# Optimization experiments

Measured on AMD Instinct MI355X. Metric: run time of the kernel, lower is better.

The kernel has to match this reference:

```python
import jax, jax.numpy as jnp
import numpy as np

Q_LO, Q_HI = 0.15, 0.85   # quantiles from __init__ q=(0.15, 0.85)
Z_INDEX = 0.0             # Z_index=0 -> mask = outside [q_lo, q_hi]
Z_SIMPLE = 1.0            # Z_index_simple fallback


def _nn_diff(S1, S2):
    # For each point in S1, signed per-coordinate residual to its nearest
    # neighbor in S2 (brute-force cdist + argmin + gather). S1:[N,3] S2:[M,3]
    d2 = (jnp.sum(S1 * S1, -1)[:, None] + jnp.sum(S2 * S2, -1)[None, :]
          - 2.0 * (S1 @ S2.T))              # [N, M] squared distances
    idx = jnp.argmin(d2, axis=1)            # nearest index in S2, [N]
    return S1 - S2[idx]                     # [N, 3]


def _robust_masked_std(x):
    # torch: quantile-based outlier mask (no_grad), then unbiased std of
    # the masked elements. Implemented with mask weights so shapes are static.
    xf = x.reshape(-1)
    xs = jax.lax.stop_gradient(xf)
    qs = jnp.quantile(xs, jnp.array([Q_LO, Q_HI], dtype=xs.dtype))
    iqr = qs[1] - qs[0]
    mask = (xs < qs[0] - Z_INDEX * iqr) | (xs > qs[1] + Z_INDEX * iqr)
    # fallback chain matching torch edge cases: simple |x-mean|>Z*std, then all
    mu, sd = xs.mean(), xs.std(ddof=1)
    simple = jnp.abs(xs - mu) > Z_SIMPLE * sd
    simple = jnp.where(simple.sum() > 0, simple, jnp.ones_like(simple))
    w = jnp.where(mask.sum() > 0, mask, simple).astype(xf.dtype)
    cnt = w.sum()
    mean_w = jnp.sum(w * xf) / cnt
    var = jnp.sum(w * (xf - mean_w) ** 2) / (cnt - 1.0)  # unbiased (torch.std)
    return jnp.sqrt(var)


def _sigma_max(S1, S2):
    s1 = _robust_masked_std(_nn_diff(S1, S2))  # std of S1->S2 residuals
    s2 = _robust_masked_std(_nn_diff(S2, S1))  # std of S2->S1 residuals
    return jnp.maximum(s1, s2)                 # max(self.sigma_distance(...))


def setup_inputs() -> dict:
    key = jax.random.key(0)
    k1, k2 = jax.random.split(key)
    B, N, M, D = 16, 4096, 4096, 3
    x = jax.random.uniform(k1, (B, N, D), dtype=jnp.float32)
    y = jax.random.uniform(k2, (B, M, D), dtype=jnp.float32)
    return {"x": x, "y": y}


def reference(x, y):
    per_batch = jax.vmap(_sigma_max)(x, y)  # [B]
    return per_batch.mean()
```

## Files before the change

kernel.cpp:

```cpp
#include <hip/hip_runtime.h>
#include <stdint.h>
#include <math.h>

typedef unsigned short u16;
typedef unsigned long long ull;

#define NPTS  4096
#define NB    16
#define NRES  12288
#define NPAIR 32
#define G     16
#define NCELL 4096
#define HCEL  0.0625f
#define SSTR  4160
#define MARGIN 1e-5f
#define RANK_LO 1843u
#define RANK_HI 10443u

__device__ __forceinline__ uint32_t f2key(float f) {
    uint32_t u = __float_as_uint(f);
    return (u & 0x80000000u) ? ~u : (u | 0x80000000u);
}
__device__ __forceinline__ float key2f(uint32_t k) {
    uint32_t u = (k & 0x80000000u) ? (k ^ 0x80000000u) : ~k;
    return __uint_as_float(u);
}

__global__ __launch_bounds__(1024) void build_kernel(const float* __restrict__ x,
                                                     const float* __restrict__ y,
                                                     float4* __restrict__ arrA,
                                                     u16* __restrict__ starts,
                                                     unsigned int* __restrict__ counters) {
    __shared__ uint32_t hist[NCELL];
    __shared__ uint32_t wpart[16];
    const int pd = blockIdx.x, b = pd >> 1, dir = pd & 1;
    const float* t = (dir == 0 ? y : x) + (size_t)b * NPTS * 3;
    const int tid = threadIdx.x, lane = tid & 63, wv = tid >> 6;

    #pragma unroll
    for (int j = 0; j < 4; ++j) hist[tid * 4 + j] = 0u;
    if (pd == 0 && tid == 0) counters[0] = 0u;
    __syncthreads();

    float f[12];
    int ci[4];
    {
        const float4* tp = reinterpret_cast<const float4*>(t + (size_t)tid * 12);
        #pragma unroll
        for (int j = 0; j < 3; ++j) {
            const float4 v = tp[j];
            f[j * 4 + 0] = v.x; f[j * 4 + 1] = v.y; f[j * 4 + 2] = v.z; f[j * 4 + 3] = v.w;
        }
        #pragma unroll
        for (int k = 0; k < 4; ++k) {
            const int cx = (int)(f[k * 3 + 0] * 16.f);
            const int cy = (int)(f[k * 3 + 1] * 16.f);
            const int cz = (int)(f[k * 3 + 2] * 16.f);
            ci[k] = (cx * G + cy) * G + cz;
            atomicAdd(&hist[ci[k]], 1u);
        }
    }
    __syncthreads();

    {
        uint32_t loc[4], sum = 0;
        const int base = tid * 4;
        #pragma unroll
        for (int j = 0; j < 4; ++j) { loc[j] = hist[base + j]; sum += loc[j]; }
        uint32_t sc = sum;
        #pragma unroll
        for (int off = 1; off < 64; off <<= 1) {
            const uint32_t u = __shfl_up(sc, off);
            if (lane >= off) sc += u;
        }
        if (lane == 63) wpart[wv] = sc;
        __syncthreads();
        uint32_t wbase = 0;
        #pragma unroll
        for (int k = 0; k < 16; ++k) wbase += (k < wv) ? wpart[k] : 0u;
        uint32_t ex = wbase + sc - sum;
        #pragma unroll
        for (int j = 0; j < 4; ++j) { hist[base + j] = ex; ex += loc[j]; }
    }
    __syncthreads();

    for (int i = tid; i <= NCELL; i += 1024)
        starts[(size_t)pd * SSTR + i] = (u16)((i == NCELL) ? NPTS : hist[i]);
    __syncthreads();

    #pragma unroll
    for (int k = 0; k < 4; ++k) {
        const float px = f[k * 3 + 0], py = f[k * 3 + 1], pz = f[k * 3 + 2];
        const uint32_t pos = atomicAdd(&hist[ci[k]], 1u);
        const float w = fmaf(pz, pz, fmaf(py, py, px * px));
        arrA[(size_t)pd * NPTS + pos] = make_float4(-2.f * px, -2.f * py, -2.f * pz, w);
    }
}

__global__ __launch_bounds__(256, 8) void query_kernel(const float4* __restrict__ arrA,
                                                       const u16* __restrict__ starts,
                                                       uint32_t* __restrict__ keys,
                                                       double* __restrict__ partials) {
    __shared__ double wred[8];
    const int pd = blockIdx.y;
    const int tid = threadIdx.x, lane = tid & 63, wv = tid >> 6;
    const int l4 = tid & 3;
    const int p = blockIdx.x * 64 + (tid >> 2);

    const float4* __restrict__ tp = arrA + (size_t)pd * NPTS;
    const u16* __restrict__ st = starts + (size_t)pd * SSTR;

    const float4 Q = arrA[(size_t)(pd ^ 1) * NPTS + p];
    const float qx = -0.5f * Q.x, qy = -0.5f * Q.y, qz = -0.5f * Q.z;
    const float qq = Q.w;
    const int cx = (int)(qx * 16.f), cy = (int)(qy * 16.f), cz = (int)(qz * 16.f);

    ull pk = ~0ull;

    {
        const int zlo = max(cz - 1, 0), zhi = min(cz + 1, G - 1);
        #define RUNB(RR, AV, NV)                                                  \
            int AV, NV;                                                           \
            { const int ix = min(max(cx + (RR) / 3 - 1, 0), G - 1);               \
              const int iy = min(max(cy + (RR) % 3 - 1, 0), G - 1);               \
              const int cc = (ix * G + iy) * G;                                   \
              AV = st[cc + zlo];                                                  \
              NV = st[cc + zhi + 1] - AV; }
        RUNB(0, a0, n0) RUNB(1, a1, n1) RUNB(2, a2, n2)
        RUNB(3, a3, n3) RUNB(4, a4, n4) RUNB(5, a5, n5)
        RUNB(6, a6, n6) RUNB(7, a7, n7) RUNB(8, a8, n8)
        #undef RUNB
        const int nc = n0 + n1 + n2 + n3 + n4 + n5 + n6 + n7 + n8;

        for (int li = l4; li < nc; li += 4) {
            int pos;
            {
                int rem = li; pos = a0 + rem;
                rem -= n0; pos = (rem >= 0) ? a1 + rem : pos;
                rem -= n1; pos = (rem >= 0) ? a2 + rem : pos;
                rem -= n2; pos = (rem >= 0) ? a3 + rem : pos;
                rem -= n3; pos = (rem >= 0) ? a4 + rem : pos;
                rem -= n4; pos = (rem >= 0) ? a5 + rem : pos;
                rem -= n5; pos = (rem >= 0) ? a6 + rem : pos;
                rem -= n6; pos = (rem >= 0) ? a7 + rem : pos;
                rem -= n7; pos = (rem >= 0) ? a8 + rem : pos;
                pos = min(pos, NPTS - 1);
            }
            const float4 T = tp[pos];
            const float d = fmaf(qx, T.x, fmaf(qy, T.y, fmaf(qz, T.z, T.w)));
            const ull cand = ((ull)f2key(d) << 32) | (uint32_t)pos;
            pk = (cand < pk) ? cand : pk;
        }
    }

    {
        ull o = __shfl_xor(pk, 1); pk = (o < pk) ? o : pk;
        o = __shfl_xor(pk, 2);     pk = (o < pk) ? o : pk;
    }

    for (int s = 2; s <= G - 1; ++s) {
        const float bd = key2f((uint32_t)(pk >> 32));
        const float dmin = (float)(s - 1) * HCEL;
        if (fmaf(dmin, dmin, -(bd + qq)) > MARGIN) break;
        for (int dx = -s; dx <= s; ++dx) {
            const int ix = cx + dx;
            if (ix < 0 || ix > G - 1) continue;
            const int adx = dx < 0 ? -dx : dx;
            for (int dy = -s; dy <= s; ++dy) {
                const int iy = cy + dy;
                if (iy < 0 || iy > G - 1) continue;
                const int ady = dy < 0 ? -dy : dy;
                const int c0 = (ix * G + iy) * G;
                #define SCANS(A_, E_)                                                 \
                    for (int p2 = (A_) + l4; p2 < (E_); p2 += 4) {                    \
                        const float4 T = tp[p2];                                      \
                        const float d = fmaf(qx, T.x, fmaf(qy, T.y,                   \
                                             fmaf(qz, T.z, T.w)));                    \
                        const ull cand = ((ull)f2key(d) << 32) | (uint32_t)p2;        \
                        pk = (cand < pk) ? cand : pk;                                 \
                    }
                if (max(adx, ady) == s) {
                    const int zl = max(cz - s, 0), zh = min(cz + s, G - 1);
                    const int a = st[c0 + zl], e = st[c0 + zh + 1];
                    SCANS(a, e)
                } else {
                    const int z1 = cz - s;
                    if (z1 >= 0) { const int a = st[c0 + z1], e = st[c0 + z1 + 1]; SCANS(a, e) }
                    const int z2 = cz + s;
                    if (z2 <= G - 1) { const int a = st[c0 + z2], e = st[c0 + z2 + 1]; SCANS(a, e) }
                }
                #undef SCANS
            }
        }
        ull o = __shfl_xor(pk, 1); pk = (o < pk) ? o : pk;
        o = __shfl_xor(pk, 2);     pk = (o < pk) ? o : pk;
    }

    const int pos = (int)(uint32_t)pk;
    const float4 T = tp[pos];
    const float rx = qx - (-0.5f * T.x);
    const float ry = qy - (-0.5f * T.y);
    const float rz = qz - (-0.5f * T.z);

    if (l4 < 3) {
        const uint32_t kk = (l4 == 0) ? f2key(rx) : ((l4 == 1) ? f2key(ry) : f2key(rz));
        keys[(size_t)pd * NRES + (size_t)p * 3 + l4] = kk;
    }

    double s1 = 0.0, s2 = 0.0;
    if (l4 == 0) {
        s1 = (double)rx + (double)ry + (double)rz;
        s2 = (double)rx * rx + (double)ry * ry + (double)rz * rz;
    }
    #pragma unroll
    for (int off = 32; off; off >>= 1) { s1 += __shfl_down(s1, off); s2 += __shfl_down(s2, off); }
    if (lane == 0) { wred[wv] = s1; wred[4 + wv] = s2; }
    __syncthreads();
    if (tid == 0) {
        double a = 0.0, c = 0.0;
        for (int k = 0; k < 4; ++k) { a += wred[k]; c += wred[4 + k]; }
        partials[(size_t)pd * 128 + blockIdx.x + 0]  = a;
        partials[(size_t)pd * 128 + 64 + blockIdx.x] = c;
    }
}

template <int BPT>
__device__ __forceinline__ void scanB(uint32_t* h, uint32_t* wtmp) {
    const int tid = threadIdx.x, lane = tid & 63, wv = tid >> 6;
    const int base = tid * BPT;
    uint32_t loc[BPT], sum = 0;
    #pragma unroll
    for (int j = 0; j < BPT; ++j) { loc[j] = h[base + j]; sum += loc[j]; }
    uint32_t sc = sum;
    #pragma unroll
    for (int off = 1; off < 64; off <<= 1) {
        const uint32_t u = __shfl_up(sc, off);
        if (lane >= off) sc += u;
    }
    if (lane == 63) wtmp[wv] = sc;
    __syncthreads();
    uint32_t wb = 0;
    #pragma unroll
    for (int k = 0; k < 16; ++k) wb += (k < wv) ? wtmp[k] : 0u;
    uint32_t ex = wb + sc - sum;
    #pragma unroll
    for (int j = 0; j < BPT; ++j) { h[base + j] = ex; ex += loc[j]; }
    __syncthreads();
}

template <int BPT>
__device__ __forceinline__ void psearchB(const uint32_t* h, int n, uint32_t r,
                                         uint32_t total, uint32_t* out3) {
    const int base = threadIdx.x * BPT;
    #pragma unroll
    for (int j = 0; j < BPT; ++j) {
        const int i = base + j;
        if (i < n) {
            const uint32_t lo = h[i];
            const uint32_t hi = (i + 1 < n) ? h[i + 1] : total;
            if (lo <= r && r < hi) { out3[0] = (uint32_t)i; out3[1] = lo; out3[2] = hi; }
        }
    }
}

__global__ __launch_bounds__(1024) void sigma_kernel(const uint32_t* __restrict__ keysg,
                                                     const double* __restrict__ partials,
                                                     float* __restrict__ sig,
                                                     unsigned int* __restrict__ counters,
                                                     float* __restrict__ out) {
    __shared__ uint32_t hist[4096];
    __shared__ uint32_t wtmp[16];
    __shared__ uint32_t bc[12];
    __shared__ double dr[64];
    __shared__ int io[32];
    __shared__ uint32_t um[32];

    const int pair = blockIdx.x;
    const int tid = threadIdx.x, lane = tid & 63, wv = tid >> 6;

    uint32_t key[12];
    const uint32_t* kp = keysg + (size_t)pair * NRES;
    #pragma unroll
    for (int e = 0; e < 12; ++e) key[e] = kp[e * 1024 + tid];

    {
        double a = (tid < 128) ? partials[(size_t)pair * 128 + tid] : 0.0;
        #pragma unroll
        for (int off = 32; off; off >>= 1) a += __shfl_down(a, off);
        if (lane == 0 && wv < 2) dr[wv] = a;
    }
    __syncthreads();
    const double S = dr[0], S2 = dr[1];
    const double mu = S / NRES;
    const double var_all = (S2 - S * mu) / (NRES - 1);
    const double sd = sqrt(var_all > 0.0 ? var_all : 0.0);
    __syncthreads();

    hist[tid * 2] = 0u; hist[tid * 2 + 1] = 0u;
    __syncthreads();
    #pragma unroll
    for (int e = 0; e < 12; ++e) atomicAdd(&hist[key[e] >> 21], 1u);
    __syncthreads();
    scanB<2>(hist, wtmp);
    psearchB<2>(hist, 2048, RANK_LO, NRES, bc + 0);
    psearchB<2>(hist, 2048, RANK_HI, NRES, bc + 3);
    __syncthreads();
    const uint32_t pA1 = bc[0], rA1 = RANK_LO - bc[1], totA1 = bc[2] - bc[1];
    const uint32_t pB1 = bc[3], rB1 = RANK_HI - bc[4], totB1 = bc[5] - bc[4];
    __syncthreads();

    #pragma unroll
    for (int j = 0; j < 4; ++j) hist[tid * 4 + j] = 0u;
    __syncthreads();
    #pragma unroll
    for (int e = 0; e < 12; ++e) {
        const uint32_t k = key[e];
        const uint32_t pfx = k >> 21, bin = (k >> 10) & 2047u;
        if (pfx == pA1) atomicAdd(&hist[bin], 1u);
        if (pfx == pB1) atomicAdd(&hist[2048 + bin], 1u);
    }
    __syncthreads();
    scanB<2>(hist, wtmp);
    scanB<2>(hist + 2048, wtmp);
    psearchB<2>(hist, 2048, rA1, totA1, bc + 0);
    psearchB<2>(hist + 2048, 2048, rB1, totB1, bc + 3);
    __syncthreads();
    const uint32_t pA2 = (pA1 << 11) | bc[0], rA2 = rA1 - bc[1], totA2 = bc[2] - bc[1];
    const uint32_t pB2 = (pB1 << 11) | bc[3], rB2 = rB1 - bc[4], totB2 = bc[5] - bc[4];
    __syncthreads();

    hist[tid * 2] = 0u; hist[tid * 2 + 1] = 0u;
    __syncthreads();
    #pragma unroll
    for (int e = 0; e < 12; ++e) {
        const uint32_t k = key[e];
        if ((k >> 10) == pA2) atomicAdd(&hist[k & 1023u], 1u);
        if ((k >> 10) == pB2) atomicAdd(&hist[1024 + (k & 1023u)], 1u);
    }
    __syncthreads();
    scanB<1>(hist, wtmp);
    scanB<1>(hist + 1024, wtmp);
    psearchB<1>(hist, 1024, rA2, totA2, bc + 0);
    psearchB<1>(hist + 1024, 1024, rB2, totB2, bc + 3);
    __syncthreads();
    const uint32_t k0 = (pA2 << 10) | bc[0];
    const uint32_t k2 = (pB2 << 10) | bc[3];
    const bool dup1 = (bc[2] >= rA2 + 2u);
    const bool dup3 = (bc[5] >= rB2 + 2u);

    uint32_t m1 = 0xFFFFFFFFu, m3 = 0xFFFFFFFFu;
    #pragma unroll
    for (int e = 0; e < 12; ++e) {
        const uint32_t k = key[e];
        if (k > k0 && k < m1) m1 = k;
        if (k > k2 && k < m3) m3 = k;
    }
    {
        uint32_t a = m1, c = m3;
        #pragma unroll
        for (int off = 32; off; off >>= 1) {
            const uint32_t ua = __shfl_down(a, off), uc = __shfl_down(c, off);
            a = (ua < a) ? ua : a; c = (uc < c) ? uc : c;
        }
        if (lane == 0) { um[wv] = a; um[16 + wv] = c; }
    }
    __syncthreads();
    uint32_t m1r = 0xFFFFFFFFu, m3r = 0xFFFFFFFFu;
    for (int k = 0; k < 16; ++k) {
        m1r = (um[k] < m1r) ? um[k] : m1r;
        m3r = (um[16 + k] < m3r) ? um[16 + k] : m3r;
    }
    const uint32_t k1 = dup1 ? k0 : m1r;
    const uint32_t k3 = dup3 ? k2 : m3r;

    const double vl0 = (double)key2f(k0), vl1 = (double)key2f(k1);
    const double vh0 = (double)key2f(k2), vh1 = (double)key2f(k3);
    const double fr_lo = 0.15 * (NRES - 1) - (double)RANK_LO;
    const double fr_hi = 0.85 * (NRES - 1) - (double)RANK_HI;
    const float q_lo = (float)(vl0 + fr_lo * (vl1 - vl0));
    const float q_hi = (float)(vh0 + fr_hi * (vh1 - vh0));

    int cq = 0, cs = 0;
    double sq = 0.0, ss = 0.0, sqq = 0.0, ssq = 0.0;
    #pragma unroll
    for (int e = 0; e < 12; ++e) {
        const float f = key2f(key[e]);
        const double fd = (double)f;
        if ((f < q_lo) || (f > q_hi)) { cq++; sq += fd; sqq += fd * fd; }
        if (fabs(fd - mu) > sd)       { cs++; ss += fd; ssq += fd * fd; }
    }
    {
        double a0 = sq, a1 = ss, a2 = sqq, a3 = ssq;
        int b0 = cq, b1 = cs;
        #pragma unroll
        for (int off = 32; off; off >>= 1) {
            a0 += __shfl_down(a0, off); a1 += __shfl_down(a1, off);
            a2 += __shfl_down(a2, off); a3 += __shfl_down(a3, off);
            b0 += __shfl_down(b0, off); b1 += __shfl_down(b1, off);
        }
        if (lane == 0) {
            dr[wv] = a0; dr[16 + wv] = a1; dr[32 + wv] = a2; dr[48 + wv] = a3;
            io[wv] = b0; io[16 + wv] = b1;
        }
    }
    __syncthreads();
    if (tid == 0) {
        double sq_t = 0, ss_t = 0, sqq_t = 0, ssq_t = 0;
        int cq_t = 0, cs_t = 0;
        for (int k = 0; k < 16; ++k) {
            sq_t += dr[k]; ss_t += dr[16 + k]; sqq_t += dr[32 + k]; ssq_t += dr[48 + k];
            cq_t += io[k]; cs_t += io[16 + k];
        }
        double cnt, sum, sumsq;
        if (cq_t > 0)      { cnt = cq_t;  sum = sq_t; sumsq = sqq_t; }
        else if (cs_t > 0) { cnt = cs_t;  sum = ss_t; sumsq = ssq_t; }
        else               { cnt = NRES;  sum = S;    sumsq = S2; }
        const double mean_w = sum / cnt;
        const double var = (sumsq - cnt * mean_w * mean_w) / (cnt - 1.0);
        const float sv = (float)sqrt(var > 0.0 ? var : 0.0);

        __hip_atomic_store(&sig[pair], sv, __ATOMIC_RELEASE, __HIP_MEMORY_SCOPE_AGENT);
        const unsigned prev = __hip_atomic_fetch_add(&counters[0], 1u,
                                                     __ATOMIC_ACQ_REL,
                                                     __HIP_MEMORY_SCOPE_AGENT);
        if (prev == NPAIR - 1) {
            float m = 0.f;
            for (int i = 0; i < NB; ++i) {
                const float s0 = __hip_atomic_load(&sig[2 * i], __ATOMIC_ACQUIRE,
                                                   __HIP_MEMORY_SCOPE_AGENT);
                const float s1v = __hip_atomic_load(&sig[2 * i + 1], __ATOMIC_ACQUIRE,
                                                    __HIP_MEMORY_SCOPE_AGENT);
                m += fmaxf(s0, s1v);
            }
            out[0] = m / (float)NB;
        }
    }
}

extern "C" void kernel_launch(void* const* d_in, const int* in_sizes, int n_in,
                              void* d_out, int out_size, void* d_ws, size_t ws_size,
                              hipStream_t stream) {
    const float* x = (const float*)d_in[0];
    const float* y = (const float*)d_in[1];
    char* w = (char*)d_ws;
    float4*       arrA     = (float4*)(w);
    uint32_t*     keys     = (uint32_t*)(w + 2097152);
    double*       partials = (double*)(w + 3670016);
    float*        sig      = (float*)(w + 3702784);
    unsigned int* counters = (unsigned int*)(w + 3702912);
    u16*          starts   = (u16*)(w + 3703040);

    build_kernel<<<NPAIR, 1024, 0, stream>>>(x, y, arrA, starts, counters);
    query_kernel<<<dim3(64, NPAIR), 256, 0, stream>>>(arrA, starts, keys, partials);
    sigma_kernel<<<NPAIR, 1024, 0, stream>>>(keys, partials, sig, counters,
                                             (float*)d_out);
}
```

Baseline: 109.0 us.

## Fuse grid build, NN query and sigma selection into one LDS-resident kernel

```diff
diff --git a/kernel.cpp b/kernel.cpp
--- a/kernel.cpp
+++ b/kernel.cpp
@@ -12,11 +12,18 @@
 #define G     16
 #define NCELL 4096
 #define HCEL  0.0625f
-#define SSTR  4160
 #define MARGIN 1e-5f
 #define RANK_LO 1843u
 #define RANK_HI 10443u
 
+#define OFF_TGT   0
+#define OFF_CST   65536
+#define OFF_KBUF  73856
+#define OFF_DM    123008
+#define OFF_UM    123776
+#define OFF_IM    124032
+#define SMEM_SZ   124160
+
 __device__ __forceinline__ uint32_t f2key(float f) {
     uint32_t u = __float_as_uint(f);
     return (u & 0x80000000u) ? ~u : (u | 0x80000000u);
@@ -26,29 +33,75 @@
     return __uint_as_float(u);
 }
 
-__global__ __launch_bounds__(1024) void build_kernel(const float* __restrict__ x,
+template <int BPT>
+__device__ __forceinline__ void scanB(uint32_t* h, uint32_t* wtmp) {
+    const int tid = threadIdx.x, lane = tid & 63, wv = tid >> 6;
+    const int base = tid * BPT;
+    uint32_t loc[BPT], sum = 0;
+    #pragma unroll
+    for (int j = 0; j < BPT; ++j) { loc[j] = h[base + j]; sum += loc[j]; }
+    uint32_t sc = sum;
+    #pragma unroll
+    for (int off = 1; off < 64; off <<= 1) {
+        const uint32_t u = __shfl_up(sc, off);
+        if (lane >= off) sc += u;
+    }
+    if (lane == 63) wtmp[wv] = sc;
+    __syncthreads();
+    uint32_t wb = 0;
+    #pragma unroll
+    for (int k = 0; k < 16; ++k) wb += (k < wv) ? wtmp[k] : 0u;
+    uint32_t ex = wb + sc - sum;
+    #pragma unroll
+    for (int j = 0; j < BPT; ++j) { h[base + j] = ex; ex += loc[j]; }
+    __syncthreads();
+}
+
+template <int BPT>
+__device__ __forceinline__ void psearchB(const uint32_t* h, int n, uint32_t r,
+                                         uint32_t total, uint32_t* out3) {
+    const int base = threadIdx.x * BPT;
+    #pragma unroll
+    for (int j = 0; j < BPT; ++j) {
+        const int i = base + j;
+        if (i < n) {
+            const uint32_t lo = h[i];
+            const uint32_t hi = (i + 1 < n) ? h[i + 1] : total;
+            if (lo <= r && r < hi) { out3[0] = (uint32_t)i; out3[1] = lo; out3[2] = hi; }
+        }
+    }
+}
+
+__global__ __launch_bounds__(1024) void fused_kernel(const float* __restrict__ x,
                                                      const float* __restrict__ y,
-                                                     float4* __restrict__ arrA,
-                                                     u16* __restrict__ starts,
-                                                     unsigned int* __restrict__ counters) {
-    __shared__ uint32_t hist[NCELL];
-    __shared__ uint32_t wpart[16];
+                                                     float* __restrict__ sig,
+                                                     unsigned int* __restrict__ counter,
+                                                     float* __restrict__ out) {
+    __shared__ __align__(16) char smem[SMEM_SZ];
+    float4*   tgt  = (float4*)(smem + OFF_TGT);
+    u16*      cst  = (u16*)(smem + OFF_CST);
+    uint32_t* kbuf = (uint32_t*)(smem + OFF_KBUF);
+    double*   dm   = (double*)(smem + OFF_DM);
+    uint32_t* um   = (uint32_t*)(smem + OFF_UM);
+    int*      im   = (int*)(smem + OFF_IM);
+
     const int pd = blockIdx.x, b = pd >> 1, dir = pd & 1;
-    const float* t = (dir == 0 ? y : x) + (size_t)b * NPTS * 3;
+    const float* tg = (dir == 0 ? y : x) + (size_t)b * NPTS * 3;
+    const float* qg = (dir == 0 ? x : y) + (size_t)b * NPTS * 3;
     const int tid = threadIdx.x, lane = tid & 63, wv = tid >> 6;
 
+    uint32_t* hist = kbuf;
     #pragma unroll
     for (int j = 0; j < 4; ++j) hist[tid * 4 + j] = 0u;
-    if (pd == 0 && tid == 0) counters[0] = 0u;
     __syncthreads();
 
     float f[12];
     int ci[4];
     {
-        const float4* tp = reinterpret_cast<const float4*>(t + (size_t)tid * 12);
+        const float4* tp4 = reinterpret_cast<const float4*>(tg + (size_t)tid * 12);
         #pragma unroll
         for (int j = 0; j < 3; ++j) {
-            const float4 v = tp[j];
+            const float4 v = tp4[j];
             f[j * 4 + 0] = v.x; f[j * 4 + 1] = v.y; f[j * 4 + 2] = v.z; f[j * 4 + 3] = v.w;
         }
         #pragma unroll
@@ -61,287 +114,188 @@
         }
     }
     __syncthreads();
-
-    {
-        uint32_t loc[4], sum = 0;
-        const int base = tid * 4;
-        #pragma unroll
-        for (int j = 0; j < 4; ++j) { loc[j] = hist[base + j]; sum += loc[j]; }
-        uint32_t sc = sum;
-        #pragma unroll
-        for (int off = 1; off < 64; off <<= 1) {
-            const uint32_t u = __shfl_up(sc, off);
-            if (lane >= off) sc += u;
-        }
-        if (lane == 63) wpart[wv] = sc;
-        __syncthreads();
-        uint32_t wbase = 0;
-        #pragma unroll
-        for (int k = 0; k < 16; ++k) wbase += (k < wv) ? wpart[k] : 0u;
-        uint32_t ex = wbase + sc - sum;
-        #pragma unroll
-        for (int j = 0; j < 4; ++j) { hist[base + j] = ex; ex += loc[j]; }
-    }
-    __syncthreads();
-
+    scanB<4>(hist, um);
     for (int i = tid; i <= NCELL; i += 1024)
-        starts[(size_t)pd * SSTR + i] = (u16)((i == NCELL) ? NPTS : hist[i]);
-    __syncthreads();
-
+        cst[i] = (u16)((i == NCELL) ? NPTS : hist[i]);
+    __syncthreads();
     #pragma unroll
     for (int k = 0; k < 4; ++k) {
         const float px = f[k * 3 + 0], py = f[k * 3 + 1], pz = f[k * 3 + 2];
         const uint32_t pos = atomicAdd(&hist[ci[k]], 1u);
         const float w = fmaf(pz, pz, fmaf(py, py, px * px));
-        arrA[(size_t)pd * NPTS + pos] = make_float4(-2.f * px, -2.f * py, -2.f * pz, w);
-    }
-}
-
-__global__ __launch_bounds__(256, 8) void query_kernel(const float4* __restrict__ arrA,
-                                                       const u16* __restrict__ starts,
-                                                       uint32_t* __restrict__ keys,
-                                                       double* __restrict__ partials) {
-    __shared__ double wred[8];
-    const int pd = blockIdx.y;
-    const int tid = threadIdx.x, lane = tid & 63, wv = tid >> 6;
-    const int l4 = tid & 3;
-    const int p = blockIdx.x * 64 + (tid >> 2);
-
-    const float4* __restrict__ tp = arrA + (size_t)pd * NPTS;
-    const u16* __restrict__ st = starts + (size_t)pd * SSTR;
-
-    const float4 Q = arrA[(size_t)(pd ^ 1) * NPTS + p];
-    const float qx = -0.5f * Q.x, qy = -0.5f * Q.y, qz = -0.5f * Q.z;
-    const float qq = Q.w;
-    const int cx = (int)(qx * 16.f), cy = (int)(qy * 16.f), cz = (int)(qz * 16.f);
-
-    ull pk = ~0ull;
+        tgt[pos] = make_float4(-2.f * px, -2.f * py, -2.f * pz, w);
+    }
+    __syncthreads();
+
+    const int l4 = tid & 3, qg4 = tid >> 2;
+    double s1a = 0.0, s2a = 0.0;
+
+    for (int r = 0; r < 16; ++r) {
+        const int qi = r * 256 + qg4;
+        const float qx = qg[qi * 3 + 0], qy = qg[qi * 3 + 1], qz = qg[qi * 3 + 2];
+        const float qq = fmaf(qz, qz, fmaf(qy, qy, qx * qx));
+        const int cx = (int)(qx * 16.f), cy = (int)(qy * 16.f), cz = (int)(qz * 16.f);
+
+        ull pk = ~0ull;
+        {
+            const int zlo = max(cz - 1, 0), zhi = min(cz + 1, G - 1);
+            #define RUNB(RR, AV, NV)                                              \
+                int AV, NV;                                                       \
+                { const int ix = min(max(cx + (RR) / 3 - 1, 0), G - 1);           \
+                  const int iy = min(max(cy + (RR) % 3 - 1, 0), G - 1);           \
+                  const int cc = (ix * G + iy) * G;                               \
+                  AV = cst[cc + zlo];                                             \
+                  NV = cst[cc + zhi + 1] - AV; }
+            RUNB(0, a0, n0) RUNB(1, a1, n1) RUNB(2, a2, n2)
+            RUNB(3, a3, n3) RUNB(4, a4, n4) RUNB(5, a5, n5)
+            RUNB(6, a6, n6) RUNB(7, a7, n7) RUNB(8, a8, n8)
+            #undef RUNB
+            const int nc = n0 + n1 + n2 + n3 + n4 + n5 + n6 + n7 + n8;
+            for (int li = l4; li < nc; li += 4) {
+                int pos;
+                {
+                    int rem = li; pos = a0 + rem;
+                    rem -= n0; pos = (rem >= 0) ? a1 + rem : pos;
+                    rem -= n1; pos = (rem >= 0) ? a2 + rem : pos;
+                    rem -= n2; pos = (rem >= 0) ? a3 + rem : pos;
+                    rem -= n3; pos = (rem >= 0) ? a4 + rem : pos;
+                    rem -= n4; pos = (rem >= 0) ? a5 + rem : pos;
+                    rem -= n5; pos = (rem >= 0) ? a6 + rem : pos;
+                    rem -= n6; pos = (rem >= 0) ? a7 + rem : pos;
+                    rem -= n7; pos = (rem >= 0) ? a8 + rem : pos;
+                    pos = min(pos, NPTS - 1);
+                }
+                const float4 T = tgt[pos];
+                const float d = fmaf(qx, T.x, fmaf(qy, T.y, fmaf(qz, T.z, T.w)));
+                const ull cand = ((ull)f2key(d) << 32) | (uint32_t)pos;
+                pk = (cand < pk) ? cand : pk;
+            }
+        }
+        {
+            ull o = __shfl_xor(pk, 1); pk = (o < pk) ? o : pk;
+            o = __shfl_xor(pk, 2);     pk = (o < pk) ? o : pk;
+        }
+        for (int s = 2; s <= G - 1; ++s) {
+            const float bd = key2f((uint32_t)(pk >> 32));
+            const float dmin = (float)(s - 1) * HCEL;
+            if (fmaf(dmin, dmin, -(bd + qq)) > MARGIN) break;
+            for (int dx = -s; dx <= s; ++dx) {
+                const int ix = cx + dx;
+                if (ix < 0 || ix > G - 1) continue;
+                const int adx = dx < 0 ? -dx : dx;
+                for (int dy = -s; dy <= s; ++dy) {
+                    const int iy = cy + dy;
+                    if (iy < 0 || iy > G - 1) continue;
+                    const int ady = dy < 0 ? -dy : dy;
+                    const int c0 = (ix * G + iy) * G;
+                    #define SCANS(A_, E_)                                             \
+                        for (int p2 = (A_) + l4; p2 < (E_); p2 += 4) {                \
+                            const float4 T = tgt[p2];                                 \
+                            const float d = fmaf(qx, T.x, fmaf(qy, T.y,               \
+                                                 fmaf(qz, T.z, T.w)));                \
+                            const ull cand = ((ull)f2key(d) << 32) | (uint32_t)p2;    \
+                            pk = (cand < pk) ? cand : pk;                             \
+                        }
+                    if (max(adx, ady) == s) {
+                        const int zl = max(cz - s, 0), zh = min(cz + s, G - 1);
+                        const int a = cst[c0 + zl], e = cst[c0 + zh + 1];
+                        SCANS(a, e)
+                    } else {
+                        const int z1 = cz - s;
+                        if (z1 >= 0) { const int a = cst[c0 + z1], e = cst[c0 + z1 + 1]; SCANS(a, e) }
+                        const int z2 = cz + s;
+                        if (z2 <= G - 1) { const int a = cst[c0 + z2], e = cst[c0 + z2 + 1]; SCANS(a, e) }
+                    }
+                    #undef SCANS
+                }
+            }
+            ull o = __shfl_xor(pk, 1); pk = (o < pk) ? o : pk;
+            o = __shfl_xor(pk, 2);     pk = (o < pk) ? o : pk;
+        }
+
+        const int pos = (int)(uint32_t)pk;
+        const float4 T = tgt[pos];
+        const float rx = qx - (-0.5f * T.x);
+        const float ry = qy - (-0.5f * T.y);
+        const float rz = qz - (-0.5f * T.z);
+        if (l4 < 3) {
+            const uint32_t kk = (l4 == 0) ? f2key(rx) : ((l4 == 1) ? f2key(ry) : f2key(rz));
+            kbuf[qi * 3 + l4] = kk;
+        }
+        if (l4 == 0) {
+            s1a += (double)rx + (double)ry + (double)rz;
+            s2a += (double)rx * rx + (double)ry * ry + (double)rz * rz;
+        }
+    }
 
     {
-        const int zlo = max(cz - 1, 0), zhi = min(cz + 1, G - 1);
-        #define RUNB(RR, AV, NV)                                                  \
-            int AV, NV;                                                           \
-            { const int ix = min(max(cx + (RR) / 3 - 1, 0), G - 1);               \
-              const int iy = min(max(cy + (RR) % 3 - 1, 0), G - 1);               \
-              const int cc = (ix * G + iy) * G;                                   \
-              AV = st[cc + zlo];                                                  \
-              NV = st[cc + zhi + 1] - AV; }
-        RUNB(0, a0, n0) RUNB(1, a1, n1) RUNB(2, a2, n2)
-        RUNB(3, a3, n3) RUNB(4, a4, n4) RUNB(5, a5, n5)
-        RUNB(6, a6, n6) RUNB(7, a7, n7) RUNB(8, a8, n8)
-        #undef RUNB
-        const int nc = n0 + n1 + n2 + n3 + n4 + n5 + n6 + n7 + n8;
-
-        for (int li = l4; li < nc; li += 4) {
-            int pos;
-            {
-                int rem = li; pos = a0 + rem;
-                rem -= n0; pos = (rem >= 0) ? a1 + rem : pos;
-                rem -= n1; pos = (rem >= 0) ? a2 + rem : pos;
-                rem -= n2; pos = (rem >= 0) ? a3 + rem : pos;
-                rem -= n3; pos = (rem >= 0) ? a4 + rem : pos;
-                rem -= n4; pos = (rem >= 0) ? a5 + rem : pos;
-                rem -= n5; pos = (rem >= 0) ? a6 + rem : pos;
-                rem -= n6; pos = (rem >= 0) ? a7 + rem : pos;
-                rem -= n7; pos = (rem >= 0) ? a8 + rem : pos;
-                pos = min(pos, NPTS - 1);
-            }
-            const float4 T = tp[pos];
-            const float d = fmaf(qx, T.x, fmaf(qy, T.y, fmaf(qz, T.z, T.w)));
-            const ull cand = ((ull)f2key(d) << 32) | (uint32_t)pos;
-            pk = (cand < pk) ? cand : pk;
-        }
-    }
-
-    {
-        ull o = __shfl_xor(pk, 1); pk = (o < pk) ? o : pk;
-        o = __shfl_xor(pk, 2);     pk = (o < pk) ? o : pk;
-    }
-
-    for (int s = 2; s <= G - 1; ++s) {
-        const float bd = key2f((uint32_t)(pk >> 32));
-        const float dmin = (float)(s - 1) * HCEL;
-        if (fmaf(dmin, dmin, -(bd + qq)) > MARGIN) break;
-        for (int dx = -s; dx <= s; ++dx) {
-            const int ix = cx + dx;
-            if (ix < 0 || ix > G - 1) continue;
-            const int adx = dx < 0 ? -dx : dx;
-            for (int dy = -s; dy <= s; ++dy) {
-                const int iy = cy + dy;
-                if (iy < 0 || iy > G - 1) continue;
-                const int ady = dy < 0 ? -dy : dy;
-                const int c0 = (ix * G + iy) * G;
-                #define SCANS(A_, E_)                                                 \
-                    for (int p2 = (A_) + l4; p2 < (E_); p2 += 4) {                    \
-                        const float4 T = tp[p2];                                      \
-                        const float d = fmaf(qx, T.x, fmaf(qy, T.y,                   \
-                                             fmaf(qz, T.z, T.w)));                    \
-                        const ull cand = ((ull)f2key(d) << 32) | (uint32_t)p2;        \
-                        pk = (cand < pk) ? cand : pk;                                 \
-                    }
-                if (max(adx, ady) == s) {
-                    const int zl = max(cz - s, 0), zh = min(cz + s, G - 1);
-                    const int a = st[c0 + zl], e = st[c0 + zh + 1];
-                    SCANS(a, e)
-                } else {
-                    const int z1 = cz - s;
-                    if (z1 >= 0) { const int a = st[c0 + z1], e = st[c0 + z1 + 1]; SCANS(a, e) }
-                    const int z2 = cz + s;
-                    if (z2 <= G - 1) { const int a = st[c0 + z2], e = st[c0 + z2 + 1]; SCANS(a, e) }
-                }
-                #undef SCANS
-            }
-        }
-        ull o = __shfl_xor(pk, 1); pk = (o < pk) ? o : pk;
-        o = __shfl_xor(pk, 2);     pk = (o < pk) ? o : pk;
-    }
-
-    const int pos = (int)(uint32_t)pk;
-    const float4 T = tp[pos];
-    const float rx = qx - (-0.5f * T.x);
-    const float ry = qy - (-0.5f * T.y);
-    const float rz = qz - (-0.5f * T.z);
-
-    if (l4 < 3) {
-        const uint32_t kk = (l4 == 0) ? f2key(rx) : ((l4 == 1) ? f2key(ry) : f2key(rz));
-        keys[(size_t)pd * NRES + (size_t)p * 3 + l4] = kk;
-    }
-
-    double s1 = 0.0, s2 = 0.0;
-    if (l4 == 0) {
-        s1 = (double)rx + (double)ry + (double)rz;
-        s2 = (double)rx * rx + (double)ry * ry + (double)rz * rz;
-    }
-    #pragma unroll
-    for (int off = 32; off; off >>= 1) { s1 += __shfl_down(s1, off); s2 += __shfl_down(s2, off); }
-    if (lane == 0) { wred[wv] = s1; wred[4 + wv] = s2; }
-    __syncthreads();
-    if (tid == 0) {
-        double a = 0.0, c = 0.0;
-        for (int k = 0; k < 4; ++k) { a += wred[k]; c += wred[4 + k]; }
-        partials[(size_t)pd * 128 + blockIdx.x + 0]  = a;
-        partials[(size_t)pd * 128 + 64 + blockIdx.x] = c;
-    }
-}
-
-template <int BPT>
-__device__ __forceinline__ void scanB(uint32_t* h, uint32_t* wtmp) {
-    const int tid = threadIdx.x, lane = tid & 63, wv = tid >> 6;
-    const int base = tid * BPT;
-    uint32_t loc[BPT], sum = 0;
-    #pragma unroll
-    for (int j = 0; j < BPT; ++j) { loc[j] = h[base + j]; sum += loc[j]; }
-    uint32_t sc = sum;
-    #pragma unroll
-    for (int off = 1; off < 64; off <<= 1) {
-        const uint32_t u = __shfl_up(sc, off);
-        if (lane >= off) sc += u;
-    }
-    if (lane == 63) wtmp[wv] = sc;
-    __syncthreads();
-    uint32_t wb = 0;
-    #pragma unroll
-    for (int k = 0; k < 16; ++k) wb += (k < wv) ? wtmp[k] : 0u;
-    uint32_t ex = wb + sc - sum;
-    #pragma unroll
-    for (int j = 0; j < BPT; ++j) { h[base + j] = ex; ex += loc[j]; }
-    __syncthreads();
-}
-
-template <int BPT>
-__device__ __forceinline__ void psearchB(const uint32_t* h, int n, uint32_t r,
-                                         uint32_t total, uint32_t* out3) {
-    const int base = threadIdx.x * BPT;
-    #pragma unroll
-    for (int j = 0; j < BPT; ++j) {
-        const int i = base + j;
-        if (i < n) {
-            const uint32_t lo = h[i];
-            const uint32_t hi = (i + 1 < n) ? h[i + 1] : total;
-            if (lo <= r && r < hi) { out3[0] = (uint32_t)i; out3[1] = lo; out3[2] = hi; }
-        }
-    }
-}
-
-__global__ __launch_bounds__(1024) void sigma_kernel(const uint32_t* __restrict__ keysg,
-                                                     const double* __restrict__ partials,
-                                                     float* __restrict__ sig,
-                                                     unsigned int* __restrict__ counters,
-                                                     float* __restrict__ out) {
-    __shared__ uint32_t hist[4096];
-    __shared__ uint32_t wtmp[16];
-    __shared__ uint32_t bc[12];
-    __shared__ double dr[64];
-    __shared__ int io[32];
-    __shared__ uint32_t um[32];
-
-    const int pair = blockIdx.x;
-    const int tid = threadIdx.x, lane = tid & 63, wv = tid >> 6;
-
-    uint32_t key[12];
-    const uint32_t* kp = keysg + (size_t)pair * NRES;
-    #pragma unroll
-    for (int e = 0; e < 12; ++e) key[e] = kp[e * 1024 + tid];
-
-    {
-        double a = (tid < 128) ? partials[(size_t)pair * 128 + tid] : 0.0;
+        double a = s1a, c = s2a;
         #pragma unroll
-        for (int off = 32; off; off >>= 1) a += __shfl_down(a, off);
-        if (lane == 0 && wv < 2) dr[wv] = a;
-    }
-    __syncthreads();
-    const double S = dr[0], S2 = dr[1];
+        for (int off = 32; off; off >>= 1) { a += __shfl_down(a, off); c += __shfl_down(c, off); }
+        if (lane == 0) { dm[wv] = a; dm[16 + wv] = c; }
+    }
+    __syncthreads();
+    double S = 0.0, S2 = 0.0;
+    for (int k = 0; k < 16; ++k) { S += dm[k]; S2 += dm[16 + k]; }
     const double mu = S / NRES;
     const double var_all = (S2 - S * mu) / (NRES - 1);
     const double sd = sqrt(var_all > 0.0 ? var_all : 0.0);
-    __syncthreads();
-
-    hist[tid * 2] = 0u; hist[tid * 2 + 1] = 0u;
-    __syncthreads();
-    #pragma unroll
-    for (int e = 0; e < 12; ++e) atomicAdd(&hist[key[e] >> 21], 1u);
-    __syncthreads();
-    scanB<2>(hist, wtmp);
-    psearchB<2>(hist, 2048, RANK_LO, NRES, bc + 0);
-    psearchB<2>(hist, 2048, RANK_HI, NRES, bc + 3);
-    __syncthreads();
-    const uint32_t pA1 = bc[0], rA1 = RANK_LO - bc[1], totA1 = bc[2] - bc[1];
-    const uint32_t pB1 = bc[3], rB1 = RANK_HI - bc[4], totB1 = bc[5] - bc[4];
-    __syncthreads();
-
-    #pragma unroll
-    for (int j = 0; j < 4; ++j) hist[tid * 4 + j] = 0u;
+
+    uint32_t key[12];
+    #pragma unroll
+    for (int e = 0; e < 12; ++e) key[e] = kbuf[e * 1024 + tid];
+    uint32_t* rh = (uint32_t*)(smem + OFF_TGT);
+    uint32_t* bc = um + 16;
+    uint32_t* mr = um + 28;
+    __syncthreads();
+
+    rh[tid * 2] = 0u; rh[tid * 2 + 1] = 0u;
+    __syncthreads();
+    #pragma unroll
+    for (int e = 0; e < 12; ++e) atomicAdd(&rh[key[e] >> 21], 1u);
+    __syncthreads();
+    scanB<2>(rh, um);
+    psearchB<2>(rh, 2048, RANK_LO, NRES, bc + 0);
+    psearchB<2>(rh, 2048, RANK_HI, NRES, bc + 3);
+    __syncthreads();
+    const uint32_t pA1 = bc[0], rA1 = RANK_LO - bc[1];
+    const uint32_t pB1 = bc[3], rB1 = RANK_HI - bc[4];
+    const uint32_t totA1 = bc[2] - bc[1], totB1 = bc[5] - bc[4];
+    __syncthreads();
+
+    #pragma unroll
+    for (int j = 0; j < 4; ++j) rh[tid * 4 + j] = 0u;
     __syncthreads();
     #pragma unroll
     for (int e = 0; e < 12; ++e) {
         const uint32_t k = key[e];
         const uint32_t pfx = k >> 21, bin = (k >> 10) & 2047u;
-        if (pfx == pA1) atomicAdd(&hist[bin], 1u);
-        if (pfx == pB1) atomicAdd(&hist[2048 + bin], 1u);
-    }
-    __syncthreads();
-    scanB<2>(hist, wtmp);
-    scanB<2>(hist + 2048, wtmp);
-    psearchB<2>(hist, 2048, rA1, totA1, bc + 0);
-    psearchB<2>(hist + 2048, 2048, rB1, totB1, bc + 3);
+        if (pfx == pA1) atomicAdd(&rh[bin], 1u);
+        if (pfx == pB1) atomicAdd(&rh[2048 + bin], 1u);
+    }
+    __syncthreads();
+    scanB<2>(rh, um);
+    scanB<2>(rh + 2048, um);
+    psearchB<2>(rh, 2048, rA1, totA1, bc + 0);
+    psearchB<2>(rh + 2048, 2048, rB1, totB1, bc + 3);
     __syncthreads();
     const uint32_t pA2 = (pA1 << 11) | bc[0], rA2 = rA1 - bc[1], totA2 = bc[2] - bc[1];
     const uint32_t pB2 = (pB1 << 11) | bc[3], rB2 = rB1 - bc[4], totB2 = bc[5] - bc[4];
     __syncthreads();
 
-    hist[tid * 2] = 0u; hist[tid * 2 + 1] = 0u;
+    rh[tid * 2] = 0u; rh[tid * 2 + 1] = 0u;
     __syncthreads();
     #pragma unroll
     for (int e = 0; e < 12; ++e) {
         const uint32_t k = key[e];
-        if ((k >> 10) == pA2) atomicAdd(&hist[k & 1023u], 1u);
-        if ((k >> 10) == pB2) atomicAdd(&hist[1024 + (k & 1023u)], 1u);
-    }
-    __syncthreads();
-    scanB<1>(hist, wtmp);
-    scanB<1>(hist + 1024, wtmp);
-    psearchB<1>(hist, 1024, rA2, totA2, bc + 0);
-    psearchB<1>(hist + 1024, 1024, rB2, totB2, bc + 3);
+        if ((k >> 10) == pA2) atomicAdd(&rh[k & 1023u], 1u);
+        if ((k >> 10) == pB2) atomicAdd(&rh[1024 + (k & 1023u)], 1u);
+    }
+    __syncthreads();
+    scanB<1>(rh, um);
+    scanB<1>(rh + 1024, um);
+    psearchB<1>(rh, 1024, rA2, totA2, bc + 0);
+    psearchB<1>(rh + 1024, 1024, rB2, totB2, bc + 3);
     __syncthreads();
     const uint32_t k0 = (pA2 << 10) | bc[0];
     const uint32_t k2 = (pB2 << 10) | bc[3];
@@ -362,13 +316,13 @@
             const uint32_t ua = __shfl_down(a, off), uc = __shfl_down(c, off);
             a = (ua < a) ? ua : a; c = (uc < c) ? uc : c;
         }
-        if (lane == 0) { um[wv] = a; um[16 + wv] = c; }
+        if (lane == 0) { mr[wv] = a; mr[16 + wv] = c; }
     }
     __syncthreads();
     uint32_t m1r = 0xFFFFFFFFu, m3r = 0xFFFFFFFFu;
     for (int k = 0; k < 16; ++k) {
-        m1r = (um[k] < m1r) ? um[k] : m1r;
-        m3r = (um[16 + k] < m3r) ? um[16 + k] : m3r;
+        m1r = (mr[k] < m1r) ? mr[k] : m1r;
+        m3r = (mr[16 + k] < m3r) ? mr[16 + k] : m3r;
     }
     const uint32_t k1 = dup1 ? k0 : m1r;
     const uint32_t k3 = dup3 ? k2 : m3r;
@@ -384,10 +338,10 @@
     double sq = 0.0, ss = 0.0, sqq = 0.0, ssq = 0.0;
     #pragma unroll
     for (int e = 0; e < 12; ++e) {
-        const float f = key2f(key[e]);
-        const double fd = (double)f;
-        if ((f < q_lo) || (f > q_hi)) { cq++; sq += fd; sqq += fd * fd; }
-        if (fabs(fd - mu) > sd)       { cs++; ss += fd; ssq += fd * fd; }
+        const float fv = key2f(key[e]);
+        const double fd = (double)fv;
+        if ((fv < q_lo) || (fv > q_hi)) { cq++; sq += fd; sqq += fd * fd; }
+        if (fabs(fd - mu) > sd)         { cs++; ss += fd; ssq += fd * fd; }
     }
     {
         double a0 = sq, a1 = ss, a2 = sqq, a3 = ssq;
@@ -399,8 +353,8 @@
             b0 += __shfl_down(b0, off); b1 += __shfl_down(b1, off);
         }
         if (lane == 0) {
-            dr[wv] = a0; dr[16 + wv] = a1; dr[32 + wv] = a2; dr[48 + wv] = a3;
-            io[wv] = b0; io[16 + wv] = b1;
+            dm[wv] = a0; dm[16 + wv] = a1; dm[32 + wv] = a2; dm[48 + wv] = a3;
+            im[wv] = b0; im[16 + wv] = b1;
         }
     }
     __syncthreads();
@@ -408,8 +362,8 @@
         double sq_t = 0, ss_t = 0, sqq_t = 0, ssq_t = 0;
         int cq_t = 0, cs_t = 0;
         for (int k = 0; k < 16; ++k) {
-            sq_t += dr[k]; ss_t += dr[16 + k]; sqq_t += dr[32 + k]; ssq_t += dr[48 + k];
-            cq_t += io[k]; cs_t += io[16 + k];
+            sq_t += dm[k]; ss_t += dm[16 + k]; sqq_t += dm[32 + k]; ssq_t += dm[48 + k];
+            cq_t += im[k]; cs_t += im[16 + k];
         }
         double cnt, sum, sumsq;
         if (cq_t > 0)      { cnt = cq_t;  sum = sq_t; sumsq = sqq_t; }
@@ -419,9 +373,8 @@
         const double var = (sumsq - cnt * mean_w * mean_w) / (cnt - 1.0);
         const float sv = (float)sqrt(var > 0.0 ? var : 0.0);
 
-        __hip_atomic_store(&sig[pair], sv, __ATOMIC_RELEASE, __HIP_MEMORY_SCOPE_AGENT);
-        const unsigned prev = __hip_atomic_fetch_add(&counters[0], 1u,
-                                                     __ATOMIC_ACQ_REL,
+        __hip_atomic_store(&sig[pd], sv, __ATOMIC_RELEASE, __HIP_MEMORY_SCOPE_AGENT);
+        const unsigned prev = __hip_atomic_fetch_add(counter, 1u, __ATOMIC_ACQ_REL,
                                                      __HIP_MEMORY_SCOPE_AGENT);
         if (prev == NPAIR - 1) {
             float m = 0.f;
@@ -442,16 +395,8 @@
                               hipStream_t stream) {
     const float* x = (const float*)d_in[0];
     const float* y = (const float*)d_in[1];
-    char* w = (char*)d_ws;
-    float4*       arrA     = (float4*)(w);
-    uint32_t*     keys     = (uint32_t*)(w + 2097152);
-    double*       partials = (double*)(w + 3670016);
-    float*        sig      = (float*)(w + 3702784);
-    unsigned int* counters = (unsigned int*)(w + 3702912);
-    u16*          starts   = (u16*)(w + 3703040);
-
-    build_kernel<<<NPAIR, 1024, 0, stream>>>(x, y, arrA, starts, counters);
-    query_kernel<<<dim3(64, NPAIR), 256, 0, stream>>>(arrA, starts, keys, partials);
-    sigma_kernel<<<NPAIR, 1024, 0, stream>>>(keys, partials, sig, counters,
-                                             (float*)d_out);
-}
+    float*        sig     = (float*)d_ws;
+    unsigned int* counter = (unsigned int*)((char*)d_ws + 128);
+    hipMemsetAsync(counter, 0, 4, stream);
+    fused_kernel<<<NPAIR, 1024, 0, stream>>>(x, y, sig, counter, (float*)d_out);
+}
```

After: 213.3 us. 1.96x slower.

## Fuse grid build into query kernel with per-block shared-memory target grid

Applied to the files above, without the earlier changes.

```diff
diff --git a/kernel.cpp b/kernel.cpp
--- a/kernel.cpp
+++ b/kernel.cpp
@@ -9,10 +9,11 @@
 #define NB    16
 #define NRES  12288
 #define NPAIR 32
+#define SUBS  16
+#define QPB   256
 #define G     16
 #define NCELL 4096
 #define HCEL  0.0625f
-#define SSTR  4160
 #define MARGIN 1e-5f
 #define RANK_LO 1843u
 #define RANK_HI 10443u
@@ -26,29 +27,72 @@
     return __uint_as_float(u);
 }
 
-__global__ __launch_bounds__(1024) void build_kernel(const float* __restrict__ x,
-                                                     const float* __restrict__ y,
-                                                     float4* __restrict__ arrA,
-                                                     u16* __restrict__ starts,
-                                                     unsigned int* __restrict__ counters) {
-    __shared__ uint32_t hist[NCELL];
-    __shared__ uint32_t wpart[16];
-    const int pd = blockIdx.x, b = pd >> 1, dir = pd & 1;
-    const float* t = (dir == 0 ? y : x) + (size_t)b * NPTS * 3;
+template <int BPT>
+__device__ __forceinline__ void scanB(uint32_t* h, uint32_t* wtmp) {
     const int tid = threadIdx.x, lane = tid & 63, wv = tid >> 6;
+    const int base = tid * BPT;
+    uint32_t loc[BPT], sum = 0;
+    #pragma unroll
+    for (int j = 0; j < BPT; ++j) { loc[j] = h[base + j]; sum += loc[j]; }
+    uint32_t sc = sum;
+    #pragma unroll
+    for (int off = 1; off < 64; off <<= 1) {
+        const uint32_t u = __shfl_up(sc, off);
+        if (lane >= off) sc += u;
+    }
+    if (lane == 63) wtmp[wv] = sc;
+    __syncthreads();
+    uint32_t wb = 0;
+    #pragma unroll
+    for (int k = 0; k < 16; ++k) wb += (k < wv) ? wtmp[k] : 0u;
+    uint32_t ex = wb + sc - sum;
+    #pragma unroll
+    for (int j = 0; j < BPT; ++j) { h[base + j] = ex; ex += loc[j]; }
+    __syncthreads();
+}
+
+template <int BPT>
+__device__ __forceinline__ void psearchB(const uint32_t* h, int n, uint32_t r,
+                                         uint32_t total, uint32_t* out3) {
+    const int base = threadIdx.x * BPT;
+    #pragma unroll
+    for (int j = 0; j < BPT; ++j) {
+        const int i = base + j;
+        if (i < n) {
+            const uint32_t lo = h[i];
+            const uint32_t hi = (i + 1 < n) ? h[i + 1] : total;
+            if (lo <= r && r < hi) { out3[0] = (uint32_t)i; out3[1] = lo; out3[2] = hi; }
+        }
+    }
+}
+
+__global__ __launch_bounds__(1024) void bq_kernel(const float* __restrict__ x,
+                                                  const float* __restrict__ y,
+                                                  uint32_t* __restrict__ keys,
+                                                  double* __restrict__ partials,
+                                                  unsigned int* __restrict__ counters) {
+    __shared__ __align__(16) float4 tgt[NPTS];
+    __shared__ u16 cst[NCELL + 64];
+    __shared__ uint32_t um[16];
+    __shared__ double wred[32];
+    uint32_t* hist = (uint32_t*)tgt;
+
+    const int pd = blockIdx.y, b = pd >> 1, dir = pd & 1;
+    const float* tg = (dir == 0 ? y : x) + (size_t)b * NPTS * 3;
+    const float* qg = (dir == 0 ? x : y) + (size_t)b * NPTS * 3;
+    const int tid = threadIdx.x, lane = tid & 63, wv = tid >> 6;
 
     #pragma unroll
     for (int j = 0; j < 4; ++j) hist[tid * 4 + j] = 0u;
-    if (pd == 0 && tid == 0) counters[0] = 0u;
     __syncthreads();
 
     float f[12];
     int ci[4];
     {
-        const float4* tp = reinterpret_cast<const float4*>(t + (size_t)tid * 12);
+        const float4* tp4 = reinterpret_cast<const float4*>(tg + (size_t)tid * 12);
         #pragma unroll
         for (int j = 0; j < 3; ++j) {
-            const float4 v = tp[j];
+            const float4 v = tp4[j];
             f[j * 4 + 0] = v.x; f[j * 4 + 1] = v.y; f[j * 4 + 2] = v.z; f[j * 4 + 3] = v.w;
         }
         #pragma unroll
@@ -61,77 +105,43 @@
         }
     }
     __syncthreads();
-
-    {
-        uint32_t loc[4], sum = 0;
-        const int base = tid * 4;
-        #pragma unroll
-        for (int j = 0; j < 4; ++j) { loc[j] = hist[base + j]; sum += loc[j]; }
-        uint32_t sc = sum;
-        #pragma unroll
-        for (int off = 1; off < 64; off <<= 1) {
-            const uint32_t u = __shfl_up(sc, off);
-            if (lane >= off) sc += u;
-        }
-        if (lane == 63) wpart[wv] = sc;
-        __syncthreads();
-        uint32_t wbase = 0;
-        #pragma unroll
-        for (int k = 0; k < 16; ++k) wbase += (k < wv) ? wpart[k] : 0u;
-        uint32_t ex = wbase + sc - sum;
-        #pragma unroll
-        for (int j = 0; j < 4; ++j) { hist[base + j] = ex; ex += loc[j]; }
-    }
-    __syncthreads();
-
+    scanB<4>(hist, um);
     for (int i = tid; i <= NCELL; i += 1024)
-        starts[(size_t)pd * SSTR + i] = (u16)((i == NCELL) ? NPTS : hist[i]);
-    __syncthreads();
-
+        cst[i] = (u16)((i == NCELL) ? NPTS : hist[i]);
+    __syncthreads();
+    uint32_t pos4[4];
+    #pragma unroll
+    for (int k = 0; k < 4; ++k) pos4[k] = atomicAdd(&hist[ci[k]], 1u);
+    __syncthreads();
     #pragma unroll
     for (int k = 0; k < 4; ++k) {
         const float px = f[k * 3 + 0], py = f[k * 3 + 1], pz = f[k * 3 + 2];
-        const uint32_t pos = atomicAdd(&hist[ci[k]], 1u);
         const float w = fmaf(pz, pz, fmaf(py, py, px * px));
-        arrA[(size_t)pd * NPTS + pos] = make_float4(-2.f * px, -2.f * py, -2.f * pz, w);
-    }
-}
-
-__global__ __launch_bounds__(256, 8) void query_kernel(const float4* __restrict__ arrA,
-                                                       const u16* __restrict__ starts,
-                                                       uint32_t* __restrict__ keys,
-                                                       double* __restrict__ partials) {
-    __shared__ double wred[8];
-    const int pd = blockIdx.y;
-    const int tid = threadIdx.x, lane = tid & 63, wv = tid >> 6;
+        tgt[pos4[k]] = make_float4(-2.f * px, -2.f * py, -2.f * pz, w);
+    }
+    __syncthreads();
+
     const int l4 = tid & 3;
-    const int p = blockIdx.x * 64 + (tid >> 2);
-
-    const float4* __restrict__ tp = arrA + (size_t)pd * NPTS;
-    const u16* __restrict__ st = starts + (size_t)pd * SSTR;
-
-    const float4 Q = arrA[(size_t)(pd ^ 1) * NPTS + p];
-    const float qx = -0.5f * Q.x, qy = -0.5f * Q.y, qz = -0.5f * Q.z;
-    const float qq = Q.w;
+    const int qi = blockIdx.x * QPB + (tid >> 2);
+    const float qx = qg[qi * 3 + 0], qy = qg[qi * 3 + 1], qz = qg[qi * 3 + 2];
+    const float qq = fmaf(qz, qz, fmaf(qy, qy, qx * qx));
     const int cx = (int)(qx * 16.f), cy = (int)(qy * 16.f), cz = (int)(qz * 16.f);
 
     ull pk = ~0ull;
-
     {
         const int zlo = max(cz - 1, 0), zhi = min(cz + 1, G - 1);
-        #define RUNB(RR, AV, NV)                                                  \
-            int AV, NV;                                                           \
-            { const int ix = min(max(cx + (RR) / 3 - 1, 0), G - 1);               \
-              const int iy = min(max(cy + (RR) % 3 - 1, 0), G - 1);               \
-              const int cc = (ix * G + iy) * G;                                   \
-              AV = st[cc + zlo];                                                  \
-              NV = st[cc + zhi + 1] - AV; }
+        #define RUNB(RR, AV, NV)                                              \
+            int AV, NV;                                                       \
+            { const int ix = min(max(cx + (RR) / 3 - 1, 0), G - 1);           \
+              const int iy = min(max(cy + (RR) % 3 - 1, 0), G - 1);           \
+              const int cc = (ix * G + iy) * G;                               \
+              AV = cst[cc + zlo];                                             \
+              NV = cst[cc + zhi + 1] - AV; }
         RUNB(0, a0, n0) RUNB(1, a1, n1) RUNB(2, a2, n2)
         RUNB(3, a3, n3) RUNB(4, a4, n4) RUNB(5, a5, n5)
         RUNB(6, a6, n6) RUNB(7, a7, n7) RUNB(8, a8, n8)
         #undef RUNB
         const int nc = n0 + n1 + n2 + n3 + n4 + n5 + n6 + n7 + n8;
-
         for (int li = l4; li < nc; li += 4) {
             int pos;
             {
@@ -146,18 +156,16 @@
                 rem -= n7; pos = (rem >= 0) ? a8 + rem : pos;
                 pos = min(pos, NPTS - 1);
             }
-            const float4 T = tp[pos];
+            const float4 T = tgt[pos];
             const float d = fmaf(qx, T.x, fmaf(qy, T.y, fmaf(qz, T.z, T.w)));
             const ull cand = ((ull)f2key(d) << 32) | (uint32_t)pos;
             pk = (cand < pk) ? cand : pk;
         }
     }
-
     {
         ull o = __shfl_xor(pk, 1); pk = (o < pk) ? o : pk;
         o = __shfl_xor(pk, 2);     pk = (o < pk) ? o : pk;
     }
-
     for (int s = 2; s <= G - 1; ++s) {
         const float bd = key2f((uint32_t)(pk >> 32));
         const float dmin = (float)(s - 1) * HCEL;
@@ -171,23 +179,23 @@
                 if (iy < 0 || iy > G - 1) continue;
                 const int ady = dy < 0 ? -dy : dy;
                 const int c0 = (ix * G + iy) * G;
-                #define SCANS(A_, E_)                                                 \
-                    for (int p2 = (A_) + l4; p2 < (E_); p2 += 4) {                    \
-                        const float4 T = tp[p2];                                      \
-                        const float d = fmaf(qx, T.x, fmaf(qy, T.y,                   \
-                                             fmaf(qz, T.z, T.w)));                    \
-                        const ull cand = ((ull)f2key(d) << 32) | (uint32_t)p2;        \
-                        pk = (cand < pk) ? cand : pk;                                 \
+                #define SCANS(A_, E_)                                             \
+                    for (int p2 = (A_) + l4; p2 < (E_); p2 += 4) {                \
+                        const float4 T = tgt[p2];                                 \
+                        const float d = fmaf(qx, T.x, fmaf(qy, T.y,               \
+                                             fmaf(qz, T.z, T.w)));                \
+                        const ull cand = ((ull)f2key(d) << 32) | (uint32_t)p2;    \
+                        pk = (cand < pk) ? cand : pk;                             \
                     }
                 if (max(adx, ady) == s) {
                     const int zl = max(cz - s, 0), zh = min(cz + s, G - 1);
-                    const int a = st[c0 + zl], e = st[c0 + zh + 1];
+                    const int a = cst[c0 + zl], e = cst[c0 + zh + 1];
                     SCANS(a, e)
                 } else {
                     const int z1 = cz - s;
-                    if (z1 >= 0) { const int a = st[c0 + z1], e = st[c0 + z1 + 1]; SCANS(a, e) }
+                    if (z1 >= 0) { const int a = cst[c0 + z1], e = cst[c0 + z1 + 1]; SCANS(a, e) }
                     const int z2 = cz + s;
-                    if (z2 <= G - 1) { const int a = st[c0 + z2], e = st[c0 + z2 + 1]; SCANS(a, e) }
+                    if (z2 <= G - 1) { const int a = cst[c0 + z2], e = cst[c0 + z2 + 1]; SCANS(a, e) }
                 }
                 #undef SCANS
             }
@@ -197,14 +205,13 @@
     }
 
     const int pos = (int)(uint32_t)pk;
-    const float4 T = tp[pos];
+    const float4 T = tgt[pos];
     const float rx = qx - (-0.5f * T.x);
     const float ry = qy - (-0.5f * T.y);
     const float rz = qz - (-0.5f * T.z);
-
     if (l4 < 3) {
         const uint32_t kk = (l4 == 0) ? f2key(rx) : ((l4 == 1) ? f2key(ry) : f2key(rz));
-        keys[(size_t)pd * NRES + (size_t)p * 3 + l4] = kk;
+        keys[(size_t)pd * NRES + (size_t)qi * 3 + l4] = kk;
     }
 
     double s1 = 0.0, s2 = 0.0;
@@ -214,53 +221,15 @@
     }
     #pragma unroll
     for (int off = 32; off; off >>= 1) { s1 += __shfl_down(s1, off); s2 += __shfl_down(s2, off); }
-    if (lane == 0) { wred[wv] = s1; wred[4 + wv] = s2; }
+    if (lane == 0) { wred[wv] = s1; wred[16 + wv] = s2; }
     __syncthreads();
     if (tid == 0) {
         double a = 0.0, c = 0.0;
-        for (int k = 0; k < 4; ++k) { a += wred[k]; c += wred[4 + k]; }
-        partials[(size_t)pd * 128 + blockIdx.x + 0]  = a;
-        partials[(size_t)pd * 128 + 64 + blockIdx.x] = c;
-    }
-}
-
-template <int BPT>
-__device__ __forceinline__ void scanB(uint32_t* h, uint32_t* wtmp) {
-    const int tid = threadIdx.x, lane = tid & 63, wv = tid >> 6;
-    const int base = tid * BPT;
-    uint32_t loc[BPT], sum = 0;
-    #pragma unroll
-    for (int j = 0; j < BPT; ++j) { loc[j] = h[base + j]; sum += loc[j]; }
-    uint32_t sc = sum;
-    #pragma unroll
-    for (int off = 1; off < 64; off <<= 1) {
-        const uint32_t u = __shfl_up(sc, off);
-        if (lane >= off) sc += u;
-    }
-    if (lane == 63) wtmp[wv] = sc;
-    __syncthreads();
-    uint32_t wb = 0;
-    #pragma unroll
-    for (int k = 0; k < 16; ++k) wb += (k < wv) ? wtmp[k] : 0u;
-    uint32_t ex = wb + sc - sum;
-    #pragma unroll
-    for (int j = 0; j < BPT; ++j) { h[base + j] = ex; ex += loc[j]; }
-    __syncthreads();
-}
-
-template <int BPT>
-__device__ __forceinline__ void psearchB(const uint32_t* h, int n, uint32_t r,
-                                         uint32_t total, uint32_t* out3) {
-    const int base = threadIdx.x * BPT;
-    #pragma unroll
-    for (int j = 0; j < BPT; ++j) {
-        const int i = base + j;
-        if (i < n) {
-            const uint32_t lo = h[i];
-            const uint32_t hi = (i + 1 < n) ? h[i + 1] : total;
-            if (lo <= r && r < hi) { out3[0] = (uint32_t)i; out3[1] = lo; out3[2] = hi; }
-        }
-    }
+        for (int k = 0; k < 16; ++k) { a += wred[k]; c += wred[16 + k]; }
+        partials[(size_t)pd * 32 + blockIdx.x]      = a;
+        partials[(size_t)pd * 32 + 16 + blockIdx.x] = c;
+    }
+    if (pd == 0 && blockIdx.x == 0 && tid == 1) counters[0] = 0u;
 }
 
 __global__ __launch_bounds__(1024) void sigma_kernel(const uint32_t* __restrict__ keysg,
@@ -283,11 +252,12 @@
     #pragma unroll
     for (int e = 0; e < 12; ++e) key[e] = kp[e * 1024 + tid];
 
-    {
-        double a = (tid < 128) ? partials[(size_t)pair * 128 + tid] : 0.0;
+    if (tid < 32) {
+        double a = partials[(size_t)pair * 32 + tid];
         #pragma unroll
-        for (int off = 32; off; off >>= 1) a += __shfl_down(a, off);
-        if (lane == 0 && wv < 2) dr[wv] = a;
+        for (int off = 8; off; off >>= 1) a += __shfl_down(a, off);
+        if (tid == 0)  dr[0] = a;
+        if (tid == 16) dr[1] = a;
     }
     __syncthreads();
     const double S = dr[0], S2 = dr[1];
@@ -384,10 +354,10 @@
     double sq = 0.0, ss = 0.0, sqq = 0.0, ssq = 0.0;
     #pragma unroll
     for (int e = 0; e < 12; ++e) {
-        const float f = key2f(key[e]);
-        const double fd = (double)f;
-        if ((f < q_lo) || (f > q_hi)) { cq++; sq += fd; sqq += fd * fd; }
-        if (fabs(fd - mu) > sd)       { cs++; ss += fd; ssq += fd * fd; }
+        const float fv = key2f(key[e]);
+        const double fd = (double)fv;
+        if ((fv < q_lo) || (fv > q_hi)) { cq++; sq += fd; sqq += fd * fd; }
+        if (fabs(fd - mu) > sd)         { cs++; ss += fd; ssq += fd * fd; }
     }
     {
         double a0 = sq, a1 = ss, a2 = sqq, a3 = ssq;
@@ -443,15 +413,12 @@
     const float* x = (const float*)d_in[0];
     const float* y = (const float*)d_in[1];
     char* w = (char*)d_ws;
-    float4*       arrA     = (float4*)(w);
-    uint32_t*     keys     = (uint32_t*)(w + 2097152);
-    double*       partials = (double*)(w + 3670016);
-    float*        sig      = (float*)(w + 3702784);
-    unsigned int* counters = (unsigned int*)(w + 3702912);
-    u16*          starts   = (u16*)(w + 3703040);
-
-    build_kernel<<<NPAIR, 1024, 0, stream>>>(x, y, arrA, starts, counters);
-    query_kernel<<<dim3(64, NPAIR), 256, 0, stream>>>(arrA, starts, keys, partials);
+    uint32_t*     keys     = (uint32_t*)(w);
+    double*       partials = (double*)(w + 1572864);
+    float*        sig      = (float*)(w + 1581056);
+    unsigned int* counters = (unsigned int*)(w + 1581184);
+
+    bq_kernel<<<dim3(SUBS, NPAIR), 1024, 0, stream>>>(x, y, keys, partials, counters);
     sigma_kernel<<<NPAIR, 1024, 0, stream>>>(keys, partials, sig, counters,
                                              (float*)d_out);
 }
```

Measured after the change: 99.81 us. 1.09x faster.
